# Kernel tuning notes

Hardware: AMD Instinct MI355X
Metric: run time of the kernel (lower is better)

## Reference

```python
import jax, jax.numpy as jnp
import numpy as np

N_NODES = 50000
N_EDGES = 400000
D_IN, D_HID, D_LAT = 1024, 512, 256


def setup_inputs() -> dict:
    key = jax.random.key(0)
    k = jax.random.split(key, 6)
    x = jax.random.normal(k[0], (N_NODES, D_IN), dtype=jnp.float32)
    edge_index = jax.random.randint(k[1], (2, N_EDGES), 0, N_NODES, dtype=jnp.int32)
    # normalized adjacency weights (e.g., D^-1/2 A D^-1/2 values), positive
    edge_weight = jax.random.uniform(k[2], (N_EDGES,), dtype=jnp.float32)
    # Glorot-style init as in GCNConv.reset_parameters
    W1 = jax.random.normal(k[3], (D_IN, D_HID), dtype=jnp.float32) * (1.0 / np.sqrt(D_IN))
    b1 = jnp.zeros((D_HID,), dtype=jnp.float32)
    W2 = jax.random.normal(k[4], (D_HID, D_LAT), dtype=jnp.float32) * (1.0 / np.sqrt(D_HID))
    b2 = jnp.zeros((D_LAT,), dtype=jnp.float32)
    return {"x": x, "edge_index": edge_index, "edge_weight": edge_weight,
            "W1": W1, "b1": b1, "W2": W2, "b2": b2}


def _gcn_layer(h, src, dst, w, W, b):
    # GCNConv: spmm(adj, h @ W) + b
    s = h @ W                                   # [N, D_out] dense GEMM
    msg = s[src] * w[:, None]                   # [E, D_out] gather + scale
    agg = jax.ops.segment_sum(msg, dst, num_segments=N_NODES)  # scatter-add
    return agg + b


def reference(x, edge_index, edge_weight, W1, b1, W2, b2):
    # eval mode: F.dropout(training=False) is identity
    src, dst = edge_index[0], edge_index[1]
    h = jax.nn.relu(_gcn_layer(x, src, dst, edge_weight, W1, b1))
    out = jax.nn.relu(_gcn_layer(h, src, dst, edge_weight, W2, b2))
    return out
```

## Files before the change

### kernel.cpp

```cpp
#include <hip/hip_runtime.h>

typedef __attribute__((ext_vector_type(8))) short short8;
typedef __attribute__((ext_vector_type(4))) float floatx4;

#define GLOBAL_AS __attribute__((address_space(1)))
#define LDS_AS __attribute__((address_space(3)))

__device__ __forceinline__ void gload_lds16(const void* g, void* l) {
  __builtin_amdgcn_global_load_lds((const GLOBAL_AS unsigned int*)g,
                                   (LDS_AS unsigned int*)l, 16, 0, 0);
}

__device__ __forceinline__ unsigned short rnbf(float f) {
  unsigned int v = __builtin_bit_cast(unsigned int, f);
  return (unsigned short)((v + 0x7fff + ((v >> 16) & 1)) >> 16);
}
__device__ __forceinline__ float bflo(unsigned int u) {
  return __builtin_bit_cast(float, u << 16);
}
__device__ __forceinline__ float bfhi(unsigned int u) {
  return __builtin_bit_cast(float, u & 0xffff0000u);
}

#define TM 128
#define TN 128
#define BKE 64

__global__ __launch_bounds__(256) void gemm_bf16(
    const unsigned short* __restrict__ A,
    const unsigned short* __restrict__ Bt,
    unsigned short* __restrict__ C,
    int M, int N, int K) {
  __shared__ __align__(16) unsigned short As[TM * BKE];
  __shared__ __align__(16) unsigned short Bs[TN * BKE];

  const int tid  = threadIdx.x;
  const int wave = tid >> 6;
  const int lane = tid & 63;
  const int wm = wave >> 1, wn = wave & 1;
  const int l15 = lane & 15, quad = lane >> 4;

  const int nwg = gridDim.x * gridDim.y;
  const int bid = blockIdx.y * gridDim.x + blockIdx.x;
  const int q = nwg >> 3, r = nwg & 7;
  const int xcd = bid & 7, off = bid >> 3;
  const int lid = ((xcd < r) ? xcd * (q + 1) : r * (q + 1) + (xcd - r) * q) + off;
  const int bm = (lid / gridDim.x) * TM;
  const int bn = (lid % gridDim.x) * TN;

  floatx4 acc[4][4];
#pragma unroll
  for (int i = 0; i < 4; ++i)
#pragma unroll
    for (int j = 0; j < 4; ++j) acc[i][j] = (floatx4){0.f, 0.f, 0.f, 0.f};

  const unsigned short* aptr[4];
  const unsigned short* bptr[4];
  int ldsoff[4];
#pragma unroll
  for (int j = 0; j < 4; ++j) {
    int ci = (wave * 4 + j) * 64 + lane;
    int rr = ci >> 3;
    int cs = (ci & 7) ^ (rr & 7);
    int arow = bm + rr; if (arow >= M) arow = M - 1;
    aptr[j] = A  + (size_t)arow * K + cs * 8;
    bptr[j] = Bt + (size_t)(bn + rr) * K + cs * 8;
    ldsoff[j] = (wave * 4 + j) * 64 * 8;
  }

  for (int k0 = 0; k0 < K; k0 += BKE) {
#pragma unroll
    for (int j = 0; j < 4; ++j) {
      gload_lds16(aptr[j] + k0, &As[ldsoff[j]]);
      gload_lds16(bptr[j] + k0, &Bs[ldsoff[j]]);
    }
    __syncthreads();
#pragma unroll
    for (int s = 0; s < 2; ++s) {
      short8 af[4], bf[4];
#pragma unroll
      for (int mt = 0; mt < 4; ++mt) {
        int mrow = wm * 64 + mt * 16 + l15;
        int sw = (s * 4 + quad) ^ (mrow & 7);
        af[mt] = *(const short8*)&As[(mrow * 8 + sw) * 8];
      }
#pragma unroll
      for (int nt = 0; nt < 4; ++nt) {
        int nrow = wn * 64 + nt * 16 + l15;
        int sw = (s * 4 + quad) ^ (nrow & 7);
        bf[nt] = *(const short8*)&Bs[(nrow * 8 + sw) * 8];
      }
#pragma unroll
      for (int mt = 0; mt < 4; ++mt)
#pragma unroll
        for (int nt = 0; nt < 4; ++nt)
          acc[mt][nt] = __builtin_amdgcn_mfma_f32_16x16x32_bf16(
              af[mt], bf[nt], acc[mt][nt], 0, 0, 0);
    }
    __syncthreads();
  }

#pragma unroll
  for (int mt = 0; mt < 4; ++mt) {
#pragma unroll
    for (int nt = 0; nt < 4; ++nt) {
      const int col = bn + wn * 64 + nt * 16 + l15;
#pragma unroll
      for (int i = 0; i < 4; ++i) {
        const int row = bm + wm * 64 + mt * 16 + quad * 4 + i;
        if (row < M) C[(size_t)row * N + col] = rnbf(acc[mt][nt][i]);
      }
    }
  }
}

#define PRE_CAST_B 1024
#define PRE_HIST_B 512
#define PRE_W1_B 512
#define PRE_W2_B 128

__global__ __launch_bounds__(256) void pre_fused(
    const float* __restrict__ x, unsigned short* __restrict__ xb, long long n4,
    const int* __restrict__ dst, int* __restrict__ cursor, int E,
    const float* __restrict__ W1, unsigned short* __restrict__ W1t,
    const float* __restrict__ W2, unsigned short* __restrict__ W2t) {
  __shared__ float tile[32][33];
  const int b = blockIdx.x, t = threadIdx.x;
  if (b < PRE_CAST_B) {
    for (long long i = (long long)b * 256 + t; i < n4;
         i += (long long)PRE_CAST_B * 256) {
      float4 v = ((const float4*)x)[i];
      ushort4 o;
      o.x = rnbf(v.x); o.y = rnbf(v.y); o.z = rnbf(v.z); o.w = rnbf(v.w);
      ((ushort4*)xb)[i] = o;
    }
  } else if (b < PRE_CAST_B + PRE_HIST_B) {
    const int bb = b - PRE_CAST_B;
    for (int e = bb * 256 + t; e < E; e += PRE_HIST_B * 256)
      atomicAdd(&cursor[dst[e]], 1);
  } else if (b < PRE_CAST_B + PRE_HIST_B + PRE_W1_B) {
    const int id = b - (PRE_CAST_B + PRE_HIST_B);
    const int bx = (id & 15) * 32, by = (id >> 4) * 32;
    const int tx = t & 31, ty = t >> 5;
#pragma unroll
    for (int j = 0; j < 4; ++j)
      tile[ty + j * 8][tx] = W1[(size_t)(by + ty + j * 8) * 512 + bx + tx];
    __syncthreads();
#pragma unroll
    for (int j = 0; j < 4; ++j)
      W1t[(size_t)(bx + ty + j * 8) * 1024 + by + tx] = rnbf(tile[tx][ty + j * 8]);
  } else {
    const int id = b - (PRE_CAST_B + PRE_HIST_B + PRE_W1_B);
    const int bx = (id & 7) * 32, by = (id >> 3) * 32;
    const int tx = t & 31, ty = t >> 5;
#pragma unroll
    for (int j = 0; j < 4; ++j)
      tile[ty + j * 8][tx] = W2[(size_t)(by + ty + j * 8) * 256 + bx + tx];
    __syncthreads();
#pragma unroll
    for (int j = 0; j < 4; ++j)
      W2t[(size_t)(bx + ty + j * 8) * 512 + by + tx] = rnbf(tile[tx][ty + j * 8]);
  }
}

__global__ __launch_bounds__(256) void scan_partial(
    const int* __restrict__ cursor, int* __restrict__ rowptr,
    int* __restrict__ partials, int n) {
  __shared__ int wsum[4];
  const int t = threadIdx.x, ln = t & 63, wv = t >> 6;
  const int base = blockIdx.x * 1024 + t * 4;
  int4 v = {0, 0, 0, 0};
  if (base + 3 < n) {
    v = *(const int4*)(cursor + base);
  } else {
    if (base + 0 < n) v.x = cursor[base + 0];
    if (base + 1 < n) v.y = cursor[base + 1];
    if (base + 2 < n) v.z = cursor[base + 2];
    if (base + 3 < n) v.w = cursor[base + 3];
  }
  const int s = v.x + v.y + v.z + v.w;
  int inc = s;
#pragma unroll
  for (int o = 1; o < 64; o <<= 1) {
    int y = __shfl_up(inc, o, 64);
    if (ln >= o) inc += y;
  }
  if (ln == 63) wsum[wv] = inc;
  __syncthreads();
  int wpre = 0;
#pragma unroll
  for (int k = 0; k < 4; ++k) wpre += (k < wv) ? wsum[k] : 0;
  const int exc = wpre + inc - s;
  if (base + 0 < n) rowptr[base + 1] = exc + v.x;
  if (base + 1 < n) rowptr[base + 2] = exc + v.x + v.y;
  if (base + 2 < n) rowptr[base + 3] = exc + v.x + v.y + v.z;
  if (base + 3 < n) rowptr[base + 4] = exc + s;
  if (t == 0) {
    partials[blockIdx.x] = wsum[0] + wsum[1] + wsum[2] + wsum[3];
  }
}

__global__ __launch_bounds__(64) void scan_base(int* partials, int nb) {
  const int t = threadIdx.x;
  const int v = (t < nb) ? partials[t] : 0;
  int inc = v;
#pragma unroll
  for (int o = 1; o < 64; o <<= 1) {
    int y = __shfl_up(inc, o, 64);
    if (t >= o) inc += y;
  }
  if (t < nb) partials[t] = inc - v;
}

__global__ __launch_bounds__(256) void scan_apply(
    int* cursor, int* __restrict__ rowptr, const int* __restrict__ partials,
    int n) {
  const int base = blockIdx.x * 1024 + threadIdx.x * 4;
  const int p = partials[blockIdx.x];
#pragma unroll
  for (int k = 0; k < 4; ++k) {
    const int i = base + k;
    if (i < n) {
      const int cnt = cursor[i];
      const int inc = p + rowptr[i + 1];
      rowptr[i + 1] = inc;
      cursor[i] = inc - cnt;
    }
  }
  if (blockIdx.x == 0 && threadIdx.x == 0) rowptr[0] = 0;
}

__global__ __launch_bounds__(256) void fill_csr(
    const int* __restrict__ dst, const int* __restrict__ src,
    const float* __restrict__ w, int* __restrict__ cursor,
    int* __restrict__ es, float* __restrict__ ws, int E) {
  int e = blockIdx.x * blockDim.x + threadIdx.x;
  if (e < E) {
    int pos = atomicAdd(&cursor[dst[e]], 1);
    es[pos] = src[e];
    ws[pos] = w[e];
  }
}

__global__ __launch_bounds__(256) void gather1_b2b(
    const unsigned short* __restrict__ S, const int* __restrict__ es,
    const float* __restrict__ ws, const int* __restrict__ rowptr,
    const float* __restrict__ bias, unsigned short* __restrict__ out, int Nn) {
  const int tn = threadIdx.x & 63;
  const int node = blockIdx.x * 4 + (threadIdx.x >> 6);
  if (node >= Nn) return;
  const int f = tn << 3;
  float acc[8] = {};
  const int beg = rowptr[node], end = rowptr[node + 1];
  for (int b = beg; b < end; b += 64) {
    const int m = end - b;
    int   sv_l = 0;
    float w_l  = 0.f;
    if (tn < m) { sv_l = es[b + tn]; w_l = ws[b + tn]; }
    const int cnt = (m < 64) ? m : 64;
    for (int i = 0; i < cnt; ++i) {
      const int   sv = __shfl(sv_l, i, 64);
      const float ww = __shfl(w_l, i, 64);
      const uint4 u = *(const uint4*)(S + (size_t)sv * 512 + f);
      acc[0] = fmaf(bflo(u.x), ww, acc[0]);
      acc[1] = fmaf(bfhi(u.x), ww, acc[1]);
      acc[2] = fmaf(bflo(u.y), ww, acc[2]);
      acc[3] = fmaf(bfhi(u.y), ww, acc[3]);
      acc[4] = fmaf(bflo(u.z), ww, acc[4]);
      acc[5] = fmaf(bfhi(u.z), ww, acc[5]);
      acc[6] = fmaf(bflo(u.w), ww, acc[6]);
      acc[7] = fmaf(bfhi(u.w), ww, acc[7]);
    }
  }
  float r[8];
#pragma unroll
  for (int j = 0; j < 8; ++j) r[j] = fmaxf(acc[j] + bias[f + j], 0.f);
  uint4 o;
  o.x = (unsigned int)rnbf(r[0]) | ((unsigned int)rnbf(r[1]) << 16);
  o.y = (unsigned int)rnbf(r[2]) | ((unsigned int)rnbf(r[3]) << 16);
  o.z = (unsigned int)rnbf(r[4]) | ((unsigned int)rnbf(r[5]) << 16);
  o.w = (unsigned int)rnbf(r[6]) | ((unsigned int)rnbf(r[7]) << 16);
  *(uint4*)(out + (size_t)node * 512 + f) = o;
}

__global__ __launch_bounds__(256) void gather2_b2f(
    const unsigned short* __restrict__ S, const int* __restrict__ es,
    const float* __restrict__ ws, const int* __restrict__ rowptr,
    const float* __restrict__ bias, float* __restrict__ out, int Nn) {
  const int tn = threadIdx.x & 31;
  const int node = blockIdx.x * 8 + (threadIdx.x >> 5);
  if (node >= Nn) return;
  const int f = tn << 3;
  float acc[8] = {};
  const int beg = rowptr[node], end = rowptr[node + 1];
  for (int b = beg; b < end; b += 32) {
    const int m = end - b;
    int   sv_l = 0;
    float w_l  = 0.f;
    if (tn < m) { sv_l = es[b + tn]; w_l = ws[b + tn]; }
    const int cnt = (m < 32) ? m : 32;
    for (int i = 0; i < cnt; ++i) {
      const int   sv = __shfl(sv_l, i, 32);
      const float ww = __shfl(w_l, i, 32);
      const uint4 u = *(const uint4*)(S + (size_t)sv * 256 + f);
      acc[0] = fmaf(bflo(u.x), ww, acc[0]);
      acc[1] = fmaf(bfhi(u.x), ww, acc[1]);
      acc[2] = fmaf(bflo(u.y), ww, acc[2]);
      acc[3] = fmaf(bfhi(u.y), ww, acc[3]);
      acc[4] = fmaf(bflo(u.z), ww, acc[4]);
      acc[5] = fmaf(bfhi(u.z), ww, acc[5]);
      acc[6] = fmaf(bflo(u.w), ww, acc[6]);
      acc[7] = fmaf(bfhi(u.w), ww, acc[7]);
    }
  }
  float4 o1, o2;
  o1.x = fmaxf(acc[0] + bias[f + 0], 0.f);
  o1.y = fmaxf(acc[1] + bias[f + 1], 0.f);
  o1.z = fmaxf(acc[2] + bias[f + 2], 0.f);
  o1.w = fmaxf(acc[3] + bias[f + 3], 0.f);
  o2.x = fmaxf(acc[4] + bias[f + 4], 0.f);
  o2.y = fmaxf(acc[5] + bias[f + 5], 0.f);
  o2.z = fmaxf(acc[6] + bias[f + 6], 0.f);
  o2.w = fmaxf(acc[7] + bias[f + 7], 0.f);
  *(float4*)(out + (size_t)node * 256 + f) = o1;
  *(float4*)(out + (size_t)node * 256 + f + 4) = o2;
}

extern "C" void kernel_launch(void* const* d_in, const int* in_sizes, int n_in,
                              void* d_out, int out_size, void* d_ws, size_t ws_size,
                              hipStream_t stream) {
  const float* x  = (const float*)d_in[0];
  const int*   ei = (const int*)d_in[1];
  const float* ew = (const float*)d_in[2];
  const float* W1 = (const float*)d_in[3];
  const float* b1 = (const float*)d_in[4];
  const float* W2 = (const float*)d_in[5];
  const float* b2 = (const float*)d_in[6];

  const int D_IN = 1024, D_HID = 512, D_LAT = 256;
  const int Nn = in_sizes[0] / D_IN;
  const int E  = in_sizes[2];
  const int* src  = ei;
  const int* dstp = ei + E;

  char* base = (char*)d_ws;
  const size_t szA = (size_t)Nn * D_IN * 2;
  const size_t szB = (size_t)Nn * D_HID * 2;
  unsigned short* xb  = (unsigned short*)base;
  unsigned short* hb  = (unsigned short*)base;
  unsigned short* s1  = (unsigned short*)(base + szA);
  unsigned short* s2  = (unsigned short*)(base + szA);
  char* tail = base + szA + szB;
  unsigned short* W1t = (unsigned short*)tail;
  unsigned short* W2t = W1t + (size_t)D_IN * D_HID;
  int*   rowptr   = (int*)(W2t + (size_t)D_HID * D_LAT);
  int*   cursor   = rowptr + (Nn + 1);
  int*   es       = cursor + Nn;
  float* wsrt     = (float*)(es + E);
  int*   partials = (int*)(wsrt + E);

  long long n4 = (long long)Nn * D_IN / 4;
  const int nsb = (Nn + 1023) / 1024;

  hipMemsetAsync(cursor, 0, (size_t)Nn * sizeof(int), stream);
  pre_fused<<<PRE_CAST_B + PRE_HIST_B + PRE_W1_B + PRE_W2_B, 256, 0, stream>>>(
      x, xb, n4, dstp, cursor, E, W1, W1t, W2, W2t);
  scan_partial<<<nsb, 256, 0, stream>>>(cursor, rowptr, partials, Nn);
  scan_base<<<1, 64, 0, stream>>>(partials, nsb);
  scan_apply<<<nsb, 256, 0, stream>>>(cursor, rowptr, partials, Nn);
  fill_csr<<<(E + 255) / 256, 256, 0, stream>>>(dstp, src, ew, cursor, es, wsrt, E);

  dim3 g1(D_HID / TN, (Nn + TM - 1) / TM);
  gemm_bf16<<<g1, 256, 0, stream>>>(xb, W1t, s1, Nn, D_HID, D_IN);
  gather1_b2b<<<(Nn + 3) / 4, 256, 0, stream>>>(
      s1, es, wsrt, rowptr, b1, hb, Nn);

  dim3 g2(D_LAT / TN, (Nn + TM - 1) / TM);
  gemm_bf16<<<g2, 256, 0, stream>>>(hb, W2t, s2, Nn, D_LAT, D_HID);
  gather2_b2f<<<(Nn + 7) / 8, 256, 0, stream>>>(
      s2, es, wsrt, rowptr, b2, (float*)d_out, Nn);
}
```

Baseline: 572.9 us.

## Fuse CSR fill into GEMM launch and stage epilogue through LDS for vector stores

The separate fill_csr kernel is folded into the first GEMM launch as 512 extra blocks that run the atomic CSR scatter alongside the GEMM tiles. The goal is to overlap the scatter with compute and drop one launch. The GEMM epilogue now writes each wave's bf16 results into swizzled LDS and then issues 16-byte row-contiguous global stores, replacing scattered 2-byte stores. Extra blocks could compete with GEMM blocks for CUs, and the block order decides whether the fill blocks actually run concurrently with the GEMM tiles.

```diff
diff --git a/kernel.cpp b/kernel.cpp
--- a/kernel.cpp
+++ b/kernel.cpp
@@ -30,9 +30,23 @@
     const unsigned short* __restrict__ A,
     const unsigned short* __restrict__ Bt,
     unsigned short* __restrict__ C,
-    int M, int N, int K) {
+    int M, int N, int K, int gx,
+    const int* __restrict__ fdst, const int* __restrict__ fsrc,
+    const float* __restrict__ fw, int* __restrict__ fcursor,
+    int* __restrict__ fes, float* __restrict__ fws, int fE, int ngemm) {
   __shared__ __align__(16) unsigned short As[TM * BKE];
   __shared__ __align__(16) unsigned short Bs[TN * BKE];
+
+  const int bid = blockIdx.x;
+  if (bid >= ngemm) {
+    const int nfb = gridDim.x - ngemm;
+    for (int e = (bid - ngemm) * 256 + threadIdx.x; e < fE; e += nfb * 256) {
+      const int pos = atomicAdd(&fcursor[fdst[e]], 1);
+      fes[pos] = fsrc[e];
+      fws[pos] = fw[e];
+    }
+    return;
+  }
 
   const int tid  = threadIdx.x;
   const int wave = tid >> 6;
@@ -40,13 +54,12 @@
   const int wm = wave >> 1, wn = wave & 1;
   const int l15 = lane & 15, quad = lane >> 4;
 
-  const int nwg = gridDim.x * gridDim.y;
-  const int bid = blockIdx.y * gridDim.x + blockIdx.x;
+  const int nwg = ngemm;
   const int q = nwg >> 3, r = nwg & 7;
   const int xcd = bid & 7, off = bid >> 3;
   const int lid = ((xcd < r) ? xcd * (q + 1) : r * (q + 1) + (xcd - r) * q) + off;
-  const int bm = (lid / gridDim.x) * TM;
-  const int bn = (lid % gridDim.x) * TN;
+  const int bm = (lid / gx) * TM;
+  const int bn = (lid % gx) * TN;
 
   floatx4 acc[4][4];
 #pragma unroll
@@ -100,16 +113,28 @@
     __syncthreads();
   }
 
+  unsigned short* wst = &As[wave * 1024];
+  const int r0 = lane >> 2;
+  const int k0c = lane & 3;
 #pragma unroll
   for (int mt = 0; mt < 4; ++mt) {
 #pragma unroll
     for (int nt = 0; nt < 4; ++nt) {
-      const int col = bn + wn * 64 + nt * 16 + l15;
 #pragma unroll
       for (int i = 0; i < 4; ++i) {
-        const int row = bm + wm * 64 + mt * 16 + quad * 4 + i;
-        if (row < M) C[(size_t)row * N + col] = rnbf(acc[mt][nt][i]);
+        const int rr = quad * 4 + i;
+        const int cc = nt * 16 + l15;
+        wst[rr * 64 + (((cc >> 3) ^ (rr & 7)) << 3) + (cc & 7)] =
+            rnbf(acc[mt][nt][i]);
       }
+    }
+    const int row_g = bm + wm * 64 + mt * 16 + r0;
+#pragma unroll
+    for (int kk = 0; kk < 2; ++kk) {
+      const int k = k0c + kk * 4;
+      short8 v = *(const short8*)&wst[r0 * 64 + ((k ^ (r0 & 7)) << 3)];
+      if (row_g < M)
+        *(short8*)&C[(size_t)row_g * N + bn + wn * 64 + k * 8] = v;
     }
   }
 }
@@ -195,9 +220,7 @@
   if (base + 1 < n) rowptr[base + 2] = exc + v.x + v.y;
   if (base + 2 < n) rowptr[base + 3] = exc + v.x + v.y + v.z;
   if (base + 3 < n) rowptr[base + 4] = exc + s;
-  if (t == 0) {
-    partials[blockIdx.x] = wsum[0] + wsum[1] + wsum[2] + wsum[3];
-  }
+  if (t == 0) partials[blockIdx.x] = wsum[0] + wsum[1] + wsum[2] + wsum[3];
 }
 
 __global__ __launch_bounds__(64) void scan_base(int* partials, int nb) {
@@ -228,18 +251,6 @@
     }
   }
   if (blockIdx.x == 0 && threadIdx.x == 0) rowptr[0] = 0;
-}
-
-__global__ __launch_bounds__(256) void fill_csr(
-    const int* __restrict__ dst, const int* __restrict__ src,
-    const float* __restrict__ w, int* __restrict__ cursor,
-    int* __restrict__ es, float* __restrict__ ws, int E) {
-  int e = blockIdx.x * blockDim.x + threadIdx.x;
-  if (e < E) {
-    int pos = atomicAdd(&cursor[dst[e]], 1);
-    es[pos] = src[e];
-    ws[pos] = w[e];
-  }
 }
 
 __global__ __launch_bounds__(256) void gather1_b2b(
@@ -368,15 +379,22 @@
   scan_partial<<<nsb, 256, 0, stream>>>(cursor, rowptr, partials, Nn);
   scan_base<<<1, 64, 0, stream>>>(partials, nsb);
   scan_apply<<<nsb, 256, 0, stream>>>(cursor, rowptr, partials, Nn);
-  fill_csr<<<(E + 255) / 256, 256, 0, stream>>>(dstp, src, ew, cursor, es, wsrt, E);
-
-  dim3 g1(D_HID / TN, (Nn + TM - 1) / TM);
-  gemm_bf16<<<g1, 256, 0, stream>>>(xb, W1t, s1, Nn, D_HID, D_IN);
+
+  const int gx1 = D_HID / TN;
+  const int gy1 = (Nn + TM - 1) / TM;
+  const int ng1 = gx1 * gy1;
+  const int nfill = 512;
+  gemm_bf16<<<ng1 + nfill, 256, 0, stream>>>(
+      xb, W1t, s1, Nn, D_HID, D_IN, gx1,
+      dstp, src, ew, cursor, es, wsrt, E, ng1);
   gather1_b2b<<<(Nn + 3) / 4, 256, 0, stream>>>(
       s1, es, wsrt, rowptr, b1, hb, Nn);
 
-  dim3 g2(D_LAT / TN, (Nn + TM - 1) / TM);
-  gemm_bf16<<<g2, 256, 0, stream>>>(hb, W2t, s2, Nn, D_LAT, D_HID);
+  const int gx2 = D_LAT / TN;
+  const int ng2 = gx2 * gy1;
+  gemm_bf16<<<ng2, 256, 0, stream>>>(
+      hb, W2t, s2, Nn, D_LAT, D_HID, gx2,
+      nullptr, nullptr, nullptr, nullptr, nullptr, nullptr, 0, ng2);
   gather2_b2f<<<(Nn + 7) / 8, 256, 0, stream>>>(
       s2, es, wsrt, rowptr, b2, (float*)d_out, Nn);
 }
```

Result: faster. 557.4 us (-2.7%).
